# Kernel optimization log

Measured on AMD Instinct MI355X. Metric: run time of the kernel, lower is better.

The kernel has to match this reference:

```python
import jax, jax.numpy as jnp
import numpy as np

LN_EPS = 1e-5

def _layernorm(x, g, b):
    m = jnp.mean(x, axis=-1, keepdims=True)
    v = jnp.var(x, axis=-1, keepdims=True)
    return (x - m) * jax.lax.rsqrt(v + LN_EPS) * g + b

def setup_inputs() -> dict:
    key = jax.random.key(0)
    ks = jax.random.split(key, 12)
    BT, D, OH, OW = 32, 768, 28, 43
    N, NFB, NFC = 12, 1024, 256
    s = 0.02
    return {
        "roi_feature": jax.random.normal(ks[0], (BT * N, NFB), jnp.float32),
        "image_feature": jax.random.normal(ks[1], (BT, D, OH, OW), jnp.float32),
        "conv_w": jax.random.normal(ks[2], (NFC, D), jnp.float32) * s,
        "conv_b": jnp.zeros((NFC,), jnp.float32),
        "emb_w": jax.random.normal(ks[3], (NFC, NFB), jnp.float32) * s,
        "emb_b": jnp.zeros((NFC,), jnp.float32),
        "ln1_g": jnp.ones((NFC,), jnp.float32),
        "ln1_b": jnp.zeros((NFC,), jnp.float32),
        "ffn_w1": jax.random.normal(ks[4], (NFC, NFC), jnp.float32) * s,
        "ffn_b1": jnp.zeros((NFC,), jnp.float32),
        "ffn_w2": jax.random.normal(ks[5], (NFC, NFC), jnp.float32) * s,
        "ffn_b2": jnp.zeros((NFC,), jnp.float32),
        "ln2_g": jnp.ones((NFC,), jnp.float32),
        "ln2_b": jnp.zeros((NFC,), jnp.float32),
        "N": 12,
        "layer_id": 1,
    }

def reference(roi_feature, image_feature, conv_w, conv_b, emb_w, emb_b,
              ln1_g, ln1_b, ffn_w1, ffn_b1, ffn_w2, ffn_b2, ln2_g, ln2_b,
              N, layer_id):
    BT, D, OH, OW = image_feature.shape
    NFC = conv_w.shape[0]
    # 1x1 conv == channel GEMM: [BT, D, OH, OW] -> [BT, NFC, OH*OW]
    img = jnp.einsum('bchw,oc->bohw', image_feature, conv_w) + conv_b[None, :, None, None]
    img = img.reshape(BT, NFC, OH * OW)                       # [BT, NFC, P]
    # roi embedding: [BT*N, NFB] -> [BT, N, NFC]
    emb = (roi_feature @ emb_w.T + emb_b).reshape(BT, N, NFC)
    # cross-attention: logits [BT, N, P], softmax over spatial positions
    logits = jnp.einsum('bnc,bcp->bnp', emb, img)
    A = jax.nn.softmax(logits, axis=2)
    ctx = jnp.einsum('bnp,bcp->bnc', A, img).reshape(BT * N, NFC)
    # residual + LN1 (dropout is identity at inference)
    x = _layernorm(ctx + emb.reshape(BT * N, NFC), ln1_g, ln1_b)
    # FFN residual + LN2
    h = jax.nn.relu(x @ ffn_w1.T + ffn_b1) @ ffn_w2.T + ffn_b2
    return _layernorm(x + h, ln2_g, ln2_b)
```

## Files before the change

### kernel.cpp

```cpp
#include <hip/hip_runtime.h>
#include <hip/hip_bf16.h>
#include <stdint.h>

typedef __hip_bfloat16 bf16;
typedef __attribute__((ext_vector_type(8))) __bf16 frag8;
typedef __attribute__((ext_vector_type(4))) float f32x4;

#define GLDS16(gsrc, ldst)                                                        \
  __builtin_amdgcn_global_load_lds(                                               \
      (const __attribute__((address_space(1))) void*)(gsrc),                      \
      (__attribute__((address_space(3))) void*)(ldst), 16, 0, 0)

__device__ inline float wred_sum(float v) {
#pragma unroll
  for (int o = 32; o; o >>= 1) v += __shfl_down(v, o);
  return v;
}
__device__ inline float wred_max(float v) {
#pragma unroll
  for (int o = 32; o; o >>= 1) v = fmaxf(v, __shfl_down(v, o));
  return v;
}
__device__ inline unsigned short bits_of(bf16 h) { return *(unsigned short*)&h; }

__global__ __launch_bounds__(256) void convert_all(
    const float* __restrict__ s0, bf16* __restrict__ d0, int n0,
    const float* __restrict__ s1, bf16* __restrict__ d1, int n1,
    const float* __restrict__ s2, bf16* __restrict__ d2, int n2,
    const float* __restrict__ s3, bf16* __restrict__ d3, int n3,
    const float* __restrict__ s4, bf16* __restrict__ d4, int n4) {
  int i = blockIdx.x * 256 + threadIdx.x;
  if (i < n0) { d0[i] = __float2bfloat16(s0[i]); return; } i -= n0;
  if (i < n1) { d1[i] = __float2bfloat16(s1[i]); return; } i -= n1;
  if (i < n2) { d2[i] = __float2bfloat16(s2[i]); return; } i -= n2;
  if (i < n3) { d3[i] = __float2bfloat16(s3[i]); return; } i -= n3;
  if (i < n4) { d4[i] = __float2bfloat16(s4[i]); }
}

__global__ __launch_bounds__(256, 2) void conv_fused(
    const float* __restrict__ X, const bf16* __restrict__ W,
    const float* __restrict__ bias, bf16* __restrict__ img) {
  int b = blockIdx.y;
  int p0 = blockIdx.x * 64;
  __shared__ __align__(16) bf16 lA[2][256 * 32];
  __shared__ __align__(16) bf16 lB[2][64 * 32];
  int tid = threadIdx.x, w = tid >> 6, lane = tid & 63;
  int lr = lane & 15, kg = lane >> 4;
  int aro = tid >> 2, aslot = tid & 3;
  int cpair = tid >> 4, pquad = tid & 15;
  const bool edge = (p0 + 64 > 1204);

  const char* Wp = (const char*)W + (long)aro * 1536 + aslot * 16;
  const float* Xp = X + ((long)b * 768 + 2 * cpair) * 1204 + p0 + pquad;

  uint4 a0, a1, a2, a3;
  float c00, c01, c02, c03, c10, c11, c12, c13;

#define LOADK(k0)                                                                  \
  {                                                                                \
    const char* wp_ = Wp + (k0) * 2;                                               \
    a0 = *(const uint4*)(wp_);                                                     \
    a1 = *(const uint4*)(wp_ + (long)64 * 1536);                                   \
    a2 = *(const uint4*)(wp_ + (long)128 * 1536);                                  \
    a3 = *(const uint4*)(wp_ + (long)192 * 1536);                                  \
    const float* xp_ = Xp + (long)(k0) * 1204;                                     \
    if (!edge) {                                                                   \
      c00 = xp_[0];    c01 = xp_[16];   c02 = xp_[32];   c03 = xp_[48];            \
      c10 = xp_[1204]; c11 = xp_[1220]; c12 = xp_[1236]; c13 = xp_[1252];          \
    } else {                                                                       \
      bool k0_ = (p0 + pquad) < 1204, k1_ = (p0 + pquad + 16) < 1204;              \
      bool k2_ = (p0 + pquad + 32) < 1204, k3_ = (p0 + pquad + 48) < 1204;         \
      c00 = k0_ ? xp_[0] : 0.f;    c01 = k1_ ? xp_[16] : 0.f;                      \
      c02 = k2_ ? xp_[32] : 0.f;   c03 = k3_ ? xp_[48] : 0.f;                      \
      c10 = k0_ ? xp_[1204] : 0.f; c11 = k1_ ? xp_[1220] : 0.f;                    \
      c12 = k2_ ? xp_[1236] : 0.f; c13 = k3_ ? xp_[1252] : 0.f;                    \
    }                                                                              \
  }

#define PACK(x, y) ((unsigned)bits_of(__float2bfloat16(x)) |                       \
                    ((unsigned)bits_of(__float2bfloat16(y)) << 16))

#define STAGE(buf)                                                                 \
  {                                                                                \
    char* La_ = (char*)lA[buf];                                                    \
    char* Lb_ = (char*)lB[buf];                                                    \
    int sw_ = (aro & 7) << 4;                                                      \
    *(uint4*)(La_ + (((aro)*64 + aslot * 16) ^ sw_)) = a0;                         \
    *(uint4*)(La_ + (((64 + aro) * 64 + aslot * 16) ^ sw_)) = a1;                  \
    *(uint4*)(La_ + (((128 + aro) * 64 + aslot * 16) ^ sw_)) = a2;                 \
    *(uint4*)(La_ + (((192 + aro) * 64 + aslot * 16) ^ sw_)) = a3;                 \
    int p_ = pquad;                                                                \
    *(unsigned*)(Lb_ + ((p_ * 64 + cpair * 4) ^ ((p_ & 7) << 4))) = PACK(c00, c10);\
    p_ = pquad + 16;                                                               \
    *(unsigned*)(Lb_ + ((p_ * 64 + cpair * 4) ^ ((p_ & 7) << 4))) = PACK(c01, c11);\
    p_ = pquad + 32;                                                               \
    *(unsigned*)(Lb_ + ((p_ * 64 + cpair * 4) ^ ((p_ & 7) << 4))) = PACK(c02, c12);\
    p_ = pquad + 48;                                                               \
    *(unsigned*)(Lb_ + ((p_ * 64 + cpair * 4) ^ ((p_ & 7) << 4))) = PACK(c03, c13);\
  }

  f32x4 acc[4][4] = {};
  LOADK(0);
#pragma unroll 2
  for (int t = 0; t < 24; ++t) {
    int buf = t & 1;
    STAGE(buf);
    if (t < 23) LOADK((t + 1) * 32);
    __syncthreads();
    const char* La = (const char*)lA[buf];
    const char* Lb = (const char*)lB[buf];
    frag8 af[4], bv[4];
#pragma unroll
    for (int mi = 0; mi < 4; ++mi) {
      int o = w * 64 + mi * 16 + lr;
      af[mi] = *(const frag8*)(La + ((o * 64 + kg * 16) ^ ((o & 7) << 4)));
    }
#pragma unroll
    for (int ni = 0; ni < 4; ++ni) {
      int p = ni * 16 + lr;
      bv[ni] = *(const frag8*)(Lb + ((p * 64 + kg * 16) ^ ((p & 7) << 4)));
    }
#pragma unroll
    for (int mi = 0; mi < 4; ++mi)
#pragma unroll
      for (int ni = 0; ni < 4; ++ni)
        acc[mi][ni] = __builtin_amdgcn_mfma_f32_16x16x32_bf16(af[mi], bv[ni],
                                                              acc[mi][ni], 0, 0, 0);
  }
#undef LOADK
#undef PACK
#undef STAGE
#pragma unroll
  for (int mi = 0; mi < 4; ++mi)
#pragma unroll
    for (int ni = 0; ni < 4; ++ni)
#pragma unroll
      for (int j = 0; j < 4; ++j) {
        int o = w * 64 + mi * 16 + kg * 4 + j;
        int p = p0 + ni * 16 + lr;
        float v = acc[mi][ni][j] + bias[o];
        img[((long)b * 256 + o) * 1280 + p] = __float2bfloat16(v);
      }
}

template <bool RELU, bool OUT_BF16>
__global__ __launch_bounds__(64) void gemm_sm(const bf16* __restrict__ A,
                                              const bf16* __restrict__ B,
                                              void* __restrict__ C, int K,
                                              const float* __restrict__ bias) {
  int n0 = blockIdx.x * 64, m0 = blockIdx.y * 64;
  int lr = threadIdx.x & 15, kg = threadIdx.x >> 4;
  f32x4 acc[4][4] = {};
#pragma unroll 2
  for (int k0 = 0; k0 < K; k0 += 32) {
    frag8 af[4], bv[4];
#pragma unroll
    for (int mi = 0; mi < 4; ++mi)
      af[mi] = *(const frag8*)(A + (long)(m0 + mi * 16 + lr) * K + k0 + kg * 8);
#pragma unroll
    for (int ni = 0; ni < 4; ++ni)
      bv[ni] = *(const frag8*)(B + (long)(n0 + ni * 16 + lr) * K + k0 + kg * 8);
#pragma unroll
    for (int mi = 0; mi < 4; ++mi)
#pragma unroll
      for (int ni = 0; ni < 4; ++ni)
        acc[mi][ni] = __builtin_amdgcn_mfma_f32_16x16x32_bf16(af[mi], bv[ni],
                                                              acc[mi][ni], 0, 0, 0);
  }
#pragma unroll
  for (int mi = 0; mi < 4; ++mi)
#pragma unroll
    for (int ni = 0; ni < 4; ++ni)
#pragma unroll
      for (int j = 0; j < 4; ++j) {
        int row = m0 + mi * 16 + kg * 4 + j;
        int col = n0 + ni * 16 + lr;
        float v = acc[mi][ni][j] + bias[col];
        if (RELU) v = fmaxf(v, 0.f);
        long idx = (long)row * 256 + col;
        if constexpr (OUT_BF16) ((bf16*)C)[idx] = __float2bfloat16(v);
        else ((float*)C)[idx] = v;
      }
}

__global__ __launch_bounds__(256) void logits_k(const bf16* __restrict__ img,
                                                const float* __restrict__ emb,
                                                float* __restrict__ lgt) {
  int b = blockIdx.x;
  __shared__ float e[3072];
  const float* eb = emb + (long)b * 3072;
  for (int i = threadIdx.x; i < 3072; i += 256) e[i] = eb[i];
  __syncthreads();
  int p = blockIdx.y * 256 + threadIdx.x;
  if (p >= 1204) return;
  const bf16* ib = img + (long)b * 256 * 1280 + p;
  float acc[12] = {};
#pragma unroll 4
  for (int c = 0; c < 256; ++c) {
    float xv = __bfloat162float(ib[(long)c * 1280]);
#pragma unroll
    for (int n = 0; n < 12; ++n) acc[n] += e[n * 256 + c] * xv;
  }
#pragma unroll
  for (int n = 0; n < 12; ++n) lgt[((long)b * 12 + n) * 1204 + p] = acc[n];
}

__global__ __launch_bounds__(256) void softmax_k(const float* __restrict__ lgt,
                                                 bf16* __restrict__ am) {
  int b = blockIdx.x, n = blockIdx.y, tid = threadIdx.x;
  bf16* row = am + ((long)b * 16 + n) * 1280;
  if (n >= 12) {
    for (int i = tid; i < 1280; i += 256) row[i] = __float2bfloat16(0.f);
    return;
  }
  const float* lr = lgt + ((long)b * 12 + n) * 1204;
  float vals[5];
  float m = -3.0e38f;
#pragma unroll
  for (int i = 0; i < 5; ++i) {
    int pp = tid + i * 256;
    vals[i] = (pp < 1204) ? lr[pp] : -3.0e38f;
    m = fmaxf(m, vals[i]);
  }
  m = wred_max(m);
  __shared__ float rd[4];
  int w = tid >> 6, lane = tid & 63;
  if (lane == 0) rd[w] = m;
  __syncthreads();
  m = fmaxf(fmaxf(rd[0], rd[1]), fmaxf(rd[2], rd[3]));
  float s = 0.f;
#pragma unroll
  for (int i = 0; i < 5; ++i) {
    int pp = tid + i * 256;
    vals[i] = (pp < 1204) ? __expf(vals[i] - m) : 0.f;
    s += vals[i];
  }
  s = wred_sum(s);
  __syncthreads();
  if (lane == 0) rd[w] = s;
  __syncthreads();
  s = rd[0] + rd[1] + rd[2] + rd[3];
  float inv = 1.f / s;
#pragma unroll
  for (int i = 0; i < 5; ++i) {
    int pp = tid + i * 256;
    row[pp] = __float2bfloat16((pp < 1204) ? vals[i] * inv : 0.f);
  }
}

__global__ __launch_bounds__(256) void ctx_split(const bf16* __restrict__ img,
                                                 const bf16* __restrict__ am,
                                                 float* __restrict__ cpart) {
  int b = blockIdx.x, kc = blockIdx.y;
  const bf16* Ab = img + (long)b * 256 * 1280;
  const bf16* Bb = am + (long)b * 16 * 1280;
  __shared__ __align__(16) bf16 lA[256 * 32];
  __shared__ __align__(16) bf16 lB[16 * 32];
  int tid = threadIdx.x, w = tid >> 6, lane = tid & 63;
  int lr = lane & 15, kg = lane >> 4;
  f32x4 acc[4] = {};
  int kend = kc * 256 + 256;
  for (int k0 = kc * 256; k0 < kend; k0 += 32) {
#pragma unroll
    for (int i = 0; i < 4; ++i) {
      int off = w * 4096 + i * 1024 + lane * 16;
      int row = off >> 6, kb = off & 63;
      GLDS16((const char*)Ab + (long)row * 2560 + k0 * 2 + kb,
             (char*)lA + w * 4096 + i * 1024);
    }
    if (w == 0) {
      int off = lane * 16, row = off >> 6, kb = off & 63;
      GLDS16((const char*)Bb + (long)row * 2560 + k0 * 2 + kb, (char*)lB);
    }
    __syncthreads();
    frag8 bv = *(const frag8*)((const char*)lB + lr * 64 + kg * 16);
#pragma unroll
    for (int mi = 0; mi < 4; ++mi) {
      frag8 av = *(const frag8*)((const char*)lA + (w * 64 + mi * 16 + lr) * 64 + kg * 16);
      acc[mi] = __builtin_amdgcn_mfma_f32_16x16x32_bf16(av, bv, acc[mi], 0, 0, 0);
    }
    __syncthreads();
  }
  int n = lr;
  if (n < 12) {
#pragma unroll
    for (int mi = 0; mi < 4; ++mi)
#pragma unroll
      for (int j = 0; j < 4; ++j)
        cpart[((long)kc * 384 + b * 12 + n) * 256 + (w * 64 + mi * 16 + kg * 4 + j)] =
            acc[mi][j];
  }
}

__global__ __launch_bounds__(256) void ln_k(const float* __restrict__ a, int nparts,
                                            long pstride, const float* __restrict__ bb,
                                            const float* __restrict__ g,
                                            const float* __restrict__ be,
                                            float* __restrict__ of,
                                            bf16* __restrict__ ob) {
  int r = blockIdx.x, c = threadIdx.x;
  long idx = (long)r * 256 + c;
  float v = bb[idx];
  for (int q = 0; q < nparts; ++q) v += a[idx + q * pstride];
  float s = wred_sum(v);
  float s2 = wred_sum(v * v);
  __shared__ float r1[4], r2[4];
  int w = c >> 6, lane = c & 63;
  if (lane == 0) { r1[w] = s; r2[w] = s2; }
  __syncthreads();
  float st = r1[0] + r1[1] + r1[2] + r1[3];
  float s2t = r2[0] + r2[1] + r2[2] + r2[3];
  float mean = st * (1.f / 256.f);
  float var = s2t * (1.f / 256.f) - mean * mean;
  float rs = rsqrtf(var + 1e-5f);
  float y = (v - mean) * rs * g[c] + be[c];
  if (of) of[idx] = y;
  if (ob) ob[idx] = __float2bfloat16(y);
}

extern "C" void kernel_launch(void* const* d_in, const int* in_sizes, int n_in,
                              void* d_out, int out_size, void* d_ws, size_t ws_size,
                              hipStream_t stream) {
  const float* roi   = (const float*)d_in[0];
  const float* imgf  = (const float*)d_in[1];
  const float* convw = (const float*)d_in[2];
  const float* convb = (const float*)d_in[3];
  const float* embw  = (const float*)d_in[4];
  const float* embb  = (const float*)d_in[5];
  const float* ln1g  = (const float*)d_in[6];
  const float* ln1b  = (const float*)d_in[7];
  const float* w1    = (const float*)d_in[8];
  const float* b1    = (const float*)d_in[9];
  const float* w2    = (const float*)d_in[10];
  const float* b2    = (const float*)d_in[11];
  const float* ln2g  = (const float*)d_in[12];
  const float* ln2b  = (const float*)d_in[13];
  float* out = (float*)d_out;

  char* p = (char*)d_ws;
  size_t off = 0;
  auto take = [&](size_t sz) -> char* {
    char* r = p + off;
    off += (sz + 255) & ~(size_t)255;
    return r;
  };
  bf16*  img   = (bf16*)take((size_t)32 * 256 * 1280 * 2);
  bf16*  cwb   = (bf16*)take((size_t)256 * 768 * 2);
  bf16*  ewb   = (bf16*)take((size_t)256 * 1024 * 2);
  bf16*  w1b   = (bf16*)take((size_t)256 * 256 * 2);
  bf16*  w2b   = (bf16*)take((size_t)256 * 256 * 2);
  bf16*  roib  = (bf16*)take((size_t)384 * 1024 * 2);
  float* emb   = (float*)take((size_t)384 * 256 * 4);
  float* lgt   = (float*)take((size_t)384 * 1204 * 4);
  bf16*  am    = (bf16*)take((size_t)32 * 16 * 1280 * 2);
  float* cpart = (float*)take((size_t)5 * 384 * 256 * 4);
  float* x     = (float*)take((size_t)384 * 256 * 4);
  bf16*  xb    = (bf16*)take((size_t)384 * 256 * 2);
  bf16*  h1    = (bf16*)take((size_t)384 * 256 * 2);
  float* h     = (float*)take((size_t)384 * 256 * 4);

  {
    int total = 196608 + 262144 + 65536 + 65536 + 393216;
    convert_all<<<(total + 255) / 256, 256, 0, stream>>>(
        convw, cwb, 196608, embw, ewb, 262144, w1, w1b, 65536, w2, w2b, 65536,
        roi, roib, 393216);
  }
  gemm_sm<false, false><<<dim3(4, 6), 64, 0, stream>>>(roib, ewb, emb, 1024, embb);
  conv_fused<<<dim3(19, 32), 256, 0, stream>>>(imgf, cwb, convb, img);
  logits_k<<<dim3(32, 5), 256, 0, stream>>>(img, emb, lgt);
  softmax_k<<<dim3(32, 16), 256, 0, stream>>>(lgt, am);
  ctx_split<<<dim3(32, 5), 256, 0, stream>>>(img, am, cpart);
  ln_k<<<384, 256, 0, stream>>>(cpart, 5, (long)384 * 256, emb, ln1g, ln1b, x, xb);
  gemm_sm<true, true><<<dim3(4, 6), 64, 0, stream>>>(xb, w1b, h1, 256, b1);
  gemm_sm<false, false><<<dim3(4, 6), 64, 0, stream>>>(h1, w2b, h, 256, b2);
  ln_k<<<384, 256, 0, stream>>>(h, 1, 0, x, ln2g, ln2b, out, nullptr);
}
```

Baseline: 135.3 us.

## Split conv GEMM output channels across blocks to double grid parallelism

The 1x1 conv GEMM now splits its 256 output channels into two 128-channel halves via a third grid dimension, giving 1216 blocks instead of 608. Each wave computes a 64x32 tile rather than 64x64, which cuts accumulator registers and LDS. The __syncthreads is replaced with an explicit lgkmcnt wait plus s_barrier wrapped in sched_barriers, and the unroll pragma and occupancy hint are dropped. In exchange, each X (image feature) tile is now loaded and converted to bf16 twice, once per channel half, so global read traffic on the large fp32 input roughly doubles.

```diff
diff --git a/kernel.cpp b/kernel.cpp
--- a/kernel.cpp
+++ b/kernel.cpp
@@ -37,32 +37,34 @@
   if (i < n4) { d4[i] = __float2bfloat16(s4[i]); }
 }
 
-__global__ __launch_bounds__(256, 2) void conv_fused(
+__global__ __launch_bounds__(256) void conv_fused(
     const float* __restrict__ X, const bf16* __restrict__ W,
     const float* __restrict__ bias, bf16* __restrict__ img) {
   int b = blockIdx.y;
   int p0 = blockIdx.x * 64;
-  __shared__ __align__(16) bf16 lA[2][256 * 32];
+  int o0 = blockIdx.z * 128;
+  __shared__ __align__(16) bf16 lA[2][128 * 32];
   __shared__ __align__(16) bf16 lB[2][64 * 32];
   int tid = threadIdx.x, w = tid >> 6, lane = tid & 63;
+  int wm = w >> 1, wn = w & 1;
   int lr = lane & 15, kg = lane >> 4;
-  int aro = tid >> 2, aslot = tid & 3;
+  int aro = tid >> 1;
+  int abase = aro * 64 + (tid & 1) * 32;
+  int swA = (aro & 7) << 4;
   int cpair = tid >> 4, pquad = tid & 15;
   const bool edge = (p0 + 64 > 1204);
 
-  const char* Wp = (const char*)W + (long)aro * 1536 + aslot * 16;
+  const char* Wp = (const char*)W + (long)(o0 + aro) * 1536 + (tid & 1) * 32;
   const float* Xp = X + ((long)b * 768 + 2 * cpair) * 1204 + p0 + pquad;
 
-  uint4 a0, a1, a2, a3;
+  uint4 a0, a1;
   float c00, c01, c02, c03, c10, c11, c12, c13;
 
 #define LOADK(k0)                                                                  \
   {                                                                                \
     const char* wp_ = Wp + (k0) * 2;                                               \
     a0 = *(const uint4*)(wp_);                                                     \
-    a1 = *(const uint4*)(wp_ + (long)64 * 1536);                                   \
-    a2 = *(const uint4*)(wp_ + (long)128 * 1536);                                  \
-    a3 = *(const uint4*)(wp_ + (long)192 * 1536);                                  \
+    a1 = *(const uint4*)(wp_ + 16);                                                \
     const float* xp_ = Xp + (long)(k0) * 1204;                                     \
     if (!edge) {                                                                   \
       c00 = xp_[0];    c01 = xp_[16];   c02 = xp_[32];   c03 = xp_[48];            \
@@ -84,11 +86,8 @@
   {                                                                                \
     char* La_ = (char*)lA[buf];                                                    \
     char* Lb_ = (char*)lB[buf];                                                    \
-    int sw_ = (aro & 7) << 4;                                                      \
-    *(uint4*)(La_ + (((aro)*64 + aslot * 16) ^ sw_)) = a0;                         \
-    *(uint4*)(La_ + (((64 + aro) * 64 + aslot * 16) ^ sw_)) = a1;                  \
-    *(uint4*)(La_ + (((128 + aro) * 64 + aslot * 16) ^ sw_)) = a2;                 \
-    *(uint4*)(La_ + (((192 + aro) * 64 + aslot * 16) ^ sw_)) = a3;                 \
+    *(uint4*)(La_ + (abase ^ swA)) = a0;                                           \
+    *(uint4*)(La_ + ((abase + 16) ^ swA)) = a1;                                    \
     int p_ = pquad;                                                                \
     *(unsigned*)(Lb_ + ((p_ * 64 + cpair * 4) ^ ((p_ & 7) << 4))) = PACK(c00, c10);\
     p_ = pquad + 16;                                                               \
@@ -99,31 +98,33 @@
     *(unsigned*)(Lb_ + ((p_ * 64 + cpair * 4) ^ ((p_ & 7) << 4))) = PACK(c03, c13);\
   }
 
-  f32x4 acc[4][4] = {};
+  f32x4 acc[4][2] = {};
   LOADK(0);
-#pragma unroll 2
   for (int t = 0; t < 24; ++t) {
     int buf = t & 1;
     STAGE(buf);
     if (t < 23) LOADK((t + 1) * 32);
-    __syncthreads();
+    __builtin_amdgcn_sched_barrier(0);
+    asm volatile("s_waitcnt lgkmcnt(0)" ::: "memory");
+    __builtin_amdgcn_s_barrier();
+    __builtin_amdgcn_sched_barrier(0);
     const char* La = (const char*)lA[buf];
     const char* Lb = (const char*)lB[buf];
-    frag8 af[4], bv[4];
+    frag8 af[4], bv[2];
 #pragma unroll
     for (int mi = 0; mi < 4; ++mi) {
-      int o = w * 64 + mi * 16 + lr;
-      af[mi] = *(const frag8*)(La + ((o * 64 + kg * 16) ^ ((o & 7) << 4)));
-    }
-#pragma unroll
-    for (int ni = 0; ni < 4; ++ni) {
-      int p = ni * 16 + lr;
+      int r = wm * 64 + mi * 16 + lr;
+      af[mi] = *(const frag8*)(La + ((r * 64 + kg * 16) ^ ((r & 7) << 4)));
+    }
+#pragma unroll
+    for (int ni = 0; ni < 2; ++ni) {
+      int p = wn * 32 + ni * 16 + lr;
       bv[ni] = *(const frag8*)(Lb + ((p * 64 + kg * 16) ^ ((p & 7) << 4)));
     }
 #pragma unroll
     for (int mi = 0; mi < 4; ++mi)
 #pragma unroll
-      for (int ni = 0; ni < 4; ++ni)
+      for (int ni = 0; ni < 2; ++ni)
         acc[mi][ni] = __builtin_amdgcn_mfma_f32_16x16x32_bf16(af[mi], bv[ni],
                                                               acc[mi][ni], 0, 0, 0);
   }
@@ -133,11 +134,11 @@
 #pragma unroll
   for (int mi = 0; mi < 4; ++mi)
 #pragma unroll
-    for (int ni = 0; ni < 4; ++ni)
+    for (int ni = 0; ni < 2; ++ni)
 #pragma unroll
       for (int j = 0; j < 4; ++j) {
-        int o = w * 64 + mi * 16 + kg * 4 + j;
-        int p = p0 + ni * 16 + lr;
+        int o = o0 + wm * 64 + mi * 16 + kg * 4 + j;
+        int p = p0 + wn * 32 + ni * 16 + lr;
         float v = acc[mi][ni][j] + bias[o];
         img[((long)b * 256 + o) * 1280 + p] = __float2bfloat16(v);
       }
@@ -366,7 +367,7 @@
         roi, roib, 393216);
   }
   gemm_sm<false, false><<<dim3(4, 6), 64, 0, stream>>>(roib, ewb, emb, 1024, embb);
-  conv_fused<<<dim3(19, 32), 256, 0, stream>>>(imgf, cwb, convb, img);
+  conv_fused<<<dim3(19, 32, 2), 256, 0, stream>>>(imgf, cwb, convb, img);
   logits_k<<<dim3(32, 5), 256, 0, stream>>>(img, emb, lgt);
   softmax_k<<<dim3(32, 16), 256, 0, stream>>>(lgt, am);
   ctx_split<<<dim3(32, 5), 256, 0, stream>>>(img, am, cpart);
```

Measured after the change: 142.6 us. +5.4%, slower.
